# Performance work log

Measured on AMD Instinct MI355X. Metric: run time of the kernel, lower is better.

Reference implementation:

```python
import jax, jax.numpy as jnp
import numpy as np

ZC, ZS = 32, 16
NS = [16384, 4096, 1024, 256, 64]  # mesh node counts per level
K_CH = 6
DEG = 12

def _key(i):
    return jax.random.fold_in(jax.random.key(0), i)

def setup_inputs():
    d = {}
    d["x"] = jax.random.normal(_key(0), (2, 16, NS[0], 3), jnp.float32)
    enc_dims = [(6, 16), (16, 16), (16, 16), (16, 32)]
    dec_dims = [(32, 16), (16, 16), (16, 16), (16, 3)]
    i = 1
    for p, dims in (("enc", enc_dims), ("decc", dec_dims), ("decs", dec_dims)):
        for l, (fi, fo) in enumerate(dims):
            d[p + "_W" + str(l)] = 0.1 * jax.random.normal(_key(i), (K_CH, fi, fo), jnp.float32); i += 1
            if p == "enc" or l < 3:  # last decoder convs have bias=None
                d[p + "_b" + str(l)] = jnp.zeros((fo,), jnp.float32)
    nfz = NS[4] * 32  # _n_features_before_z
    d["mu_W"] = 0.1 * jax.random.normal(_key(i), (ZC + ZS, nfz), jnp.float32); i += 1
    d["mu_b"] = jnp.zeros((ZC + ZS,), jnp.float32)
    d["linc_W"] = 0.1 * jax.random.normal(_key(i), (nfz, ZC), jnp.float32); i += 1
    d["linc_b"] = jnp.zeros((nfz,), jnp.float32)
    d["lins_W"] = 0.1 * jax.random.normal(_key(i), (nfz, ZC + 2 * ZS), jnp.float32); i += 1
    d["lins_b"] = jnp.zeros((nfz,), jnp.float32)
    for l in range(4):
        d["ei" + str(l)] = jax.random.randint(_key(i), (2, DEG * NS[l]), 0, NS[l], jnp.int32); i += 1
    d["ei4"] = jax.random.randint(_key(i), (2, DEG * NS[0]), 0, NS[0], jnp.int32); i += 1
    for l in range(4):
        d["ds_i" + str(l)] = jax.random.randint(_key(i), (NS[l + 1], 3), 0, NS[l], jnp.int32); i += 1
        d["ds_w" + str(l)] = jax.random.uniform(_key(i), (NS[l + 1], 3), jnp.float32); i += 1
        d["us_i" + str(l)] = jax.random.randint(_key(i), (NS[l], 3), 0, NS[l + 1], jnp.int32); i += 1
        d["us_w" + str(l)] = jax.random.uniform(_key(i), (NS[l], 3), jnp.float32); i += 1
    return d

def _norm(ei, n):
    # ChebConv_Coma.norm: D^-1/2 A D^-1/2 edge weights (unit edge weights)
    row, col = ei[0], ei[1]
    deg = jnp.zeros((n,), jnp.float32).at[row].add(1.0)
    dis = jnp.where(deg > 0, 1.0 / jnp.sqrt(jnp.maximum(deg, 1.0)), 0.0)
    return dis[row] * dis[col]

def _prop(x, ei, w, n):
    # sparse matvec: out[:, dst] += w_e * x[:, src]   (x: [B, n, F])
    msg = x[:, ei[0], :] * w[None, :, None]
    return jnp.zeros((x.shape[0], n, x.shape[2]), x.dtype).at[:, ei[1], :].add(msg)

def _cheb(x, ei, w, Wk, b, n):
    # Chebyshev recurrence: T0=x, T1=Lx, Tk=2L T_{k-1} - T_{k-2}
    out = jnp.einsum('bnf,fg->bng', x, Wk[0])
    Tx0 = x
    Tx1 = _prop(x, ei, w, n)
    out = out + jnp.einsum('bnf,fg->bng', Tx1, Wk[1])
    for k in range(2, Wk.shape[0]):
        Tx2 = 2.0 * _prop(Tx1, ei, w, n) - Tx0
        out = out + jnp.einsum('bnf,fg->bng', Tx2, Wk[k])
        Tx0, Tx1 = Tx1, Tx2
    return out if b is None else out + b

def _pool(x, idx, w):
    # sparse pooling matrix, 3 nnz/row: out[:, i] = sum_k w[i,k] * x[:, idx[i,k]]
    return jnp.einsum('bnkf,nk->bnf', x[:, idx, :], w)

def _phase(x):
    # PhaseTensor: doubles last dim with cos/sin phase modulation over time axis 1
    T = x.shape[1]
    th = 2.0 * jnp.pi * jnp.arange(T, dtype=x.dtype) / T
    shp = (1, T) + (1,) * (x.ndim - 2)
    return jnp.concatenate([x * jnp.cos(th).reshape(shp), x * jnp.sin(th).reshape(shp)], axis=-1)

def _model(FL, IL):
    (x, eW0, eb0, eW1, eb1, eW2, eb2, eW3, eb3,
     cW0, cb0, cW1, cb1, cW2, cb2, cW3,
     sW0, sb0, sW1, sb1, sW2, sb2, sW3,
     mu_W, mu_b, linc_W, linc_b, lins_W, lins_b,
     ds_w0, ds_w1, ds_w2, ds_w3, us_w0, us_w1, us_w2, us_w3) = FL
    (ei0, ei1, ei2, ei3, ei4,
     ds_i0, ds_i1, ds_i2, ds_i3, us_i0, us_i1, us_i2, us_i3) = IL
    eis = [ei0, ei1, ei2, ei3, ei4]
    lvl_n = [NS[0], NS[1], NS[2], NS[3], NS[0]]
    nrm = [_norm(eis[l], lvl_n[l]) for l in range(5)]
    B, T, N0, F0 = x.shape
    # phase_input: [B,T,N,3] -> [B,T,N,6]; fold time into batch for the conv stack
    h = _phase(x).reshape(B * T, N0, 2 * F0)
    encW = [(eW0, eb0), (eW1, eb1), (eW2, eb2), (eW3, eb3)]
    dsl = [(ds_i0, ds_w0), (ds_i1, ds_w1), (ds_i2, ds_w2), (ds_i3, ds_w3)]
    usl = [(us_i0, us_w0), (us_i1, us_w1), (us_i2, us_w2), (us_i3, us_w3)]
    for l in range(4):
        h = jax.nn.relu(_cheb(h, eis[l], nrm[l], encW[l][0], encW[l][1], NS[l]))
        h = _pool(h, dsl[l][0], dsl[l][1])
    h = h.reshape(B, T, -1)  # [B, T, N4*32]
    mu = jnp.einsum('btf,zf->btz', h, mu_W) + mu_b
    # faithful to torch code: per-t cat along dim 0 (time-major) then reshape(-1, T, z)
    mu_c = jnp.mean(jnp.swapaxes(mu[..., :ZC], 0, 1).reshape(B, T, ZC), axis=1)
    mu_s = jnp.mean(jnp.swapaxes(mu[..., ZC:], 0, 1).reshape(B, T, ZS), axis=1)

    def dec(z, Ws, bs, lW, lb, relu_first):
        y = z @ lW.T + lb
        if relu_first:
            y = jax.nn.relu(y)
        y = y.reshape(y.shape[0], NS[4], Ws[0].shape[1])  # [*, N4, 32]
        for i in range(3):  # n_layers - 1 upsample+conv+relu
            lvl = 3 - i
            y = _pool(y, usl[lvl][0], usl[lvl][1])
            y = jax.nn.relu(_cheb(y, eis[lvl], nrm[lvl], Ws[i], bs[i], NS[lvl]))
        y = _pool(y, usl[0][0], usl[0][1])
        return _cheb(y, eis[4], nrm[4], Ws[3], None, NS[0])  # final conv, no bias/relu

    s_avg = dec(mu_c, [cW0, cW1, cW2, cW3], [cb0, cb1, cb2], linc_W, linc_b, False)
    # decoder_s, vectorized over timeframes by folding T into batch
    zs_ph = _phase(jnp.broadcast_to(mu_s[:, None, :], (B, T, ZS)))  # [B,T,2*ZS]
    zc_rep = jnp.broadcast_to(mu_c[:, None, :], (B, T, ZC))
    zin = jnp.concatenate([zc_rep, zs_ph], axis=-1).reshape(B * T, ZC + 2 * ZS)
    ds_t = dec(zin, [sW0, sW1, sW2, sW3], [sb0, sb1, sb2], lins_W, lins_b, True).reshape(B, T, N0, 3)
    s_t = s_avg[:, None] + ds_t
    return mu_c, mu_s, s_avg, s_t

def reference(x, enc_W0, enc_b0, enc_W1, enc_b1, enc_W2, enc_b2, enc_W3, enc_b3, decc_W0, decc_b0, decc_W1, decc_b1, decc_W2, decc_b2, decc_W3, decs_W0, decs_b0, decs_W1, decs_b1, decs_W2, decs_b2, decs_W3, mu_W, mu_b, linc_W, linc_b, lins_W, lins_b, ds_w0, ds_w1, ds_w2, ds_w3, us_w0, us_w1, us_w2, us_w3, ei0, ei1, ei2, ei3, ei4, ds_i0, ds_i1, ds_i2, ds_i3, us_i0, us_i1, us_i2, us_i3):
    FL = (x, enc_W0, enc_b0, enc_W1, enc_b1, enc_W2, enc_b2, enc_W3, enc_b3,
          decc_W0, decc_b0, decc_W1, decc_b1, decc_W2, decc_b2, decc_W3,
          decs_W0, decs_b0, decs_W1, decs_b1, decs_W2, decs_b2, decs_W3,
          mu_W, mu_b, linc_W, linc_b, lins_W, lins_b,
          ds_w0, ds_w1, ds_w2, ds_w3, us_w0, us_w1, us_w2, us_w3)
    IL = (ei0, ei1, ei2, ei3, ei4, ds_i0, ds_i1, ds_i2, ds_i3, us_i0, us_i1, us_i2, us_i3)
    return _model(FL, IL)
```

## Files before the change

kernel.cpp:

```cpp
#include <hip/hip_runtime.h>
#include <cstdint>
#include <cstddef>

#define TPB 256

typedef float f32x4 __attribute__((ext_vector_type(4)));
typedef float f32x2 __attribute__((ext_vector_type(2)));
typedef int   i32x4 __attribute__((ext_vector_type(4)));

static inline int cdiv(long long a, int b){ return (int)((a + (long long)b - 1) / b); }

#define NTOT 38144
#define ETOT 457728
#define CTOT 762880
#define RPTOT 38149

static hipStream_t g_s2 = nullptr;
static hipEvent_t g_evF1 = nullptr, g_evPre = nullptr, g_evF2 = nullptr, g_evDecc = nullptr;
__attribute__((constructor)) static void init_side_stream(){
  if (hipStreamCreateWithFlags(&g_s2, hipStreamNonBlocking) != hipSuccess){ g_s2 = nullptr; return; }
  if (hipEventCreateWithFlags(&g_evF1, hipEventDisableTiming) != hipSuccess ||
      hipEventCreateWithFlags(&g_evPre, hipEventDisableTiming) != hipSuccess ||
      hipEventCreateWithFlags(&g_evF2, hipEventDisableTiming) != hipSuccess ||
      hipEventCreateWithFlags(&g_evDecc, hipEventDisableTiming) != hipSuccess){
    g_s2 = nullptr;
  }
}


template<int W>
__device__ __forceinline__ void vload(const float* __restrict__ p, float* r){
  if constexpr (W == 8){ vload<4>(p, r); vload<4>(p+4, r+4); }
  else if constexpr (W == 4){ f32x4 v = *reinterpret_cast<const f32x4*>(p); r[0]=v.x;r[1]=v.y;r[2]=v.z;r[3]=v.w; }
  else { f32x2 v = *reinterpret_cast<const f32x2*>(p); r[0]=v.x;r[1]=v.y; }
}
template<int W>
__device__ __forceinline__ void vstore(float* __restrict__ p, const float* r){
  if constexpr (W == 8){ vstore<4>(p, r); vstore<4>(p+4, r+4); }
  else if constexpr (W == 4){ f32x4 v; v.x=r[0];v.y=r[1];v.z=r[2];v.w=r[3]; *reinterpret_cast<f32x4*>(p) = v; }
  else { f32x2 v; v.x=r[0];v.y=r[1]; *reinterpret_cast<f32x2*>(p) = v; }
}

template<int F>
__device__ __forceinline__ void loadrow(const float* __restrict__ p, float* r){
  #pragma unroll
  for (int q = 0; q < F/4; ++q) vload<4>(p + 4*q, r + 4*q);
}
template<int F>
__device__ __forceinline__ void storerow(float* __restrict__ p, const float* r){
  #pragma unroll
  for (int q = 0; q < F/4; ++q) vstore<4>(p + 4*q, r + 4*q);
}


__device__ __forceinline__ bool lvl_edge(int t, const int* e0,const int* e1,const int* e2,const int* e3,const int* e4,
                                         const int*& ei, int& E, int& noff, int& rpoff, int& rel){
  if (t < 196608){ ei=e0; E=196608; noff=0;     rpoff=0;     rel=t;        return true; }
  if (t < 245760){ ei=e1; E=49152;  noff=16384; rpoff=16385; rel=t-196608; return true; }
  if (t < 258048){ ei=e2; E=12288;  noff=20480; rpoff=20482; rel=t-245760; return true; }
  if (t < 261120){ ei=e3; E=3072;   noff=21504; rpoff=21507; rel=t-258048; return true; }
  if (t < 457728){ ei=e4; E=196608; noff=21760; rpoff=21764; rel=t-261120; return true; }
  return false;
}

__global__ void k_degs_all(const int* e0,const int* e1,const int* e2,const int* e3,const int* e4,
                           int* __restrict__ rowdeg, int* __restrict__ dstdeg){
  int t = blockIdx.x*blockDim.x + threadIdx.x;
  const int* ei; int E, noff, rpoff, rel;
  if (!lvl_edge(t, e0,e1,e2,e3,e4, ei,E,noff,rpoff,rel)) return;
  atomicAdd(&rowdeg[noff + ei[rel]], 1);
  atomicAdd(&dstdeg[noff + ei[E + rel]], 1);
}

__global__ void k_dis_all(const int* __restrict__ rowdeg, float* __restrict__ dis){
  int t = blockIdx.x*blockDim.x + threadIdx.x;
  if (t >= NTOT) return;
  int d = rowdeg[t];
  dis[t] = d > 0 ? rsqrtf((float)d) : 0.f;
}

__global__ void k_scan5(const int* __restrict__ dstdeg, int* __restrict__ rp, int* __restrict__ cursor){
  const int NnA[5]  = {16384,4096,1024,256,16384};
  const int NOFF[5] = {0,16384,20480,21504,21760};
  const int COFF[5] = {0,327680,409600,430080,435200};
  __shared__ int part[257];
  int l = blockIdx.x;
  int N = NnA[l];
  const int* cnt = dstdeg + NOFF[l];
  int* rpl = rp + NOFF[l] + l;
  int* cul = cursor + NOFF[l] + l;
  int tid = threadIdx.x;
  int chunk = (N + 255) / 256;
  int lo = tid*chunk; if (lo > N) lo = N;
  int hi = lo + chunk; if (hi > N) hi = N;
  int s = 0;
  for (int i = lo; i < hi; ++i) s += (cnt[i] + 7) & ~7;
  part[tid+1] = s;
  if (tid == 0) part[0] = COFF[l];
  __syncthreads();
  if (tid == 0){ for (int i = 1; i <= 256; ++i) part[i] += part[i-1]; }
  __syncthreads();
  int run = part[tid];
  for (int i = lo; i < hi; ++i){ rpl[i] = run; cul[i] = run; run += (cnt[i] + 7) & ~7; }
  if (tid == 0) rpl[N] = part[256];
}

__global__ void k_fill_all(const int* e0,const int* e1,const int* e2,const int* e3,const int* e4,
                           const float* __restrict__ dis, int* __restrict__ cursor,
                           int* __restrict__ srcs, float* __restrict__ w){
  int t = blockIdx.x*blockDim.x + threadIdx.x;
  const int* ei; int E, noff, rpoff, rel;
  if (!lvl_edge(t, e0,e1,e2,e3,e4, ei,E,noff,rpoff,rel)) return;
  int src = ei[rel], dst = ei[E + rel];
  int pos = atomicAdd(&cursor[rpoff + dst], 1);
  srcs[pos] = src;
  w[pos] = dis[noff + src] * dis[noff + dst];
}

__global__ void k_pad_all(const int* __restrict__ dstdeg, const int* __restrict__ rp,
                          int* __restrict__ srcs, float* __restrict__ w){
  int t = blockIdx.x*blockDim.x + threadIdx.x;
  if (t >= NTOT) return;
  int rpoff, n;
  if      (t < 16384){ rpoff = 0;     n = t; }
  else if (t < 20480){ rpoff = 16385; n = t - 16384; }
  else if (t < 21504){ rpoff = 20482; n = t - 20480; }
  else if (t < 21760){ rpoff = 21507; n = t - 21504; }
  else               { rpoff = 21764; n = t - 21760; }
  int j0 = rp[rpoff + n];
  int j1 = rp[rpoff + n + 1];
  int cnt = dstdeg[t];
  int sfill = cnt > 0 ? srcs[j0] : 0;
  for (int j = j0 + cnt; j < j1; ++j){ srcs[j] = sfill; w[j] = 0.f; }
}


template<int FinPad>
__device__ __forceinline__ void tmap(int N, int& gb, int& n, int& gs, int& sub, int& laneoff){
  constexpr int LPR = FinPad/4;
  gb = blockIdx.x & 7;
  int I = (blockIdx.x >> 3)*256 + threadIdx.x;
  n = I / FinPad;
  int u = I - n*FinPad;
  gs = u / LPR;
  sub = u - gs*LPR;
  laneoff = gs*FinPad + sub*4;
}

template<int FinPad>
__device__ __forceinline__ void gather8_t(const float* __restrict__ base,
                                          const int* __restrict__ srcs, const float* __restrict__ w,
                                          int j0, int j1, int laneoff, float* acc){
  constexpr int RS = 4*FinPad;
  #pragma unroll
  for (int q = 0; q < 4; ++q) acc[q] = 0.f;
  for (int j = j0; j < j1; j += 8){
    i32x4 sa = *reinterpret_cast<const i32x4*>(srcs + j);
    i32x4 sb = *reinterpret_cast<const i32x4*>(srcs + j + 4);
    f32x4 wa = *reinterpret_cast<const f32x4*>(w + j);
    f32x4 wb = *reinterpret_cast<const f32x4*>(w + j + 4);
    float v0[4], v1[4], v2[4], v3[4], v4[4], v5[4], v6[4], v7[4];
    vload<4>(base + (size_t)sa.x*RS + laneoff, v0);
    vload<4>(base + (size_t)sa.y*RS + laneoff, v1);
    vload<4>(base + (size_t)sa.z*RS + laneoff, v2);
    vload<4>(base + (size_t)sa.w*RS + laneoff, v3);
    vload<4>(base + (size_t)sb.x*RS + laneoff, v4);
    vload<4>(base + (size_t)sb.y*RS + laneoff, v5);
    vload<4>(base + (size_t)sb.z*RS + laneoff, v6);
    vload<4>(base + (size_t)sb.w*RS + laneoff, v7);
    #pragma unroll
    for (int q = 0; q < 4; ++q){
      acc[q] = fmaf(wa.x, v0[q], acc[q]);
      acc[q] = fmaf(wa.y, v1[q], acc[q]);
      acc[q] = fmaf(wa.z, v2[q], acc[q]);
      acc[q] = fmaf(wa.w, v3[q], acc[q]);
      acc[q] = fmaf(wb.x, v4[q], acc[q]);
      acc[q] = fmaf(wb.y, v5[q], acc[q]);
      acc[q] = fmaf(wb.z, v6[q], acc[q]);
      acc[q] = fmaf(wb.w, v7[q], acc[q]);
    }
  }
}

template<int FinPad, int FinReal, int Fout>
__device__ __forceinline__ void gemm_t(const float* ts, const float* __restrict__ Wk,
                                       int sub, float* o){
  constexpr int LPR = FinPad/4;
  int lane = (int)threadIdx.x & 63;
  int lanebase = lane & ~(LPR-1);
  float tv[FinPad];
  #pragma unroll
  for (int s = 0; s < LPR; ++s)
    #pragma unroll
    for (int q = 0; q < 4; ++q)
      tv[s*4+q] = __shfl(ts[q], lanebase + s, 64);
  if constexpr (Fout % 4 == 0){
    constexpr int OPL = Fout/LPR;
    #pragma unroll
    for (int fi = 0; fi < FinReal; ++fi)
      #pragma unroll
      for (int q = 0; q < OPL; ++q)
        o[q] = fmaf(tv[fi], Wk[fi*Fout + sub*OPL + q], o[q]);
  } else {
    if (sub < Fout){
      #pragma unroll
      for (int fi = 0; fi < FinReal; ++fi)
        o[0] = fmaf(tv[fi], Wk[fi*Fout + sub], o[0]);
    }
  }
}

template<int FinPad, int PRE>
__global__ void k_pre_t(const float* __restrict__ psrc, const int* __restrict__ pidx,
                        const float* __restrict__ pw, float* __restrict__ bufX,
                        int N, int Nin){
  int gb, n, gs, sub, laneoff;
  tmap<FinPad>(N, gb, n, gs, sub, laneoff);
  constexpr int RS = 4*FinPad;
  float r[4];
  if constexpr (PRE == 1){
    int g = (gb<<2) | gs;
    int t = g & 15;
    float th = 6.283185307179586f * (float)t / 16.0f;
    float sn, cs; sincosf(th, &sn, &cs);
    const float* xr = psrc + ((size_t)g*16384 + n)*3;
    #pragma unroll
    for (int q = 0; q < 4; ++q){
      int f = sub*4 + q;
      float v = 0.f;
      if (f < 6) v = xr[f % 3] * (f < 3 ? cs : sn);
      r[q] = v;
    }
  } else {
    int i0 = pidx[n*3+0], i1 = pidx[n*3+1], i2 = pidx[n*3+2];
    float w0 = pw[n*3+0], w1 = pw[n*3+1], w2 = pw[n*3+2];
    const float* pb = psrc + (size_t)gb*Nin*RS + laneoff;
    float a[4], b[4], c[4];
    vload<4>(pb + (size_t)i0*RS, a);
    vload<4>(pb + (size_t)i1*RS, b);
    vload<4>(pb + (size_t)i2*RS, c);
    #pragma unroll
    for (int q = 0; q < 4; ++q) r[q] = fmaf(w0, a[q], fmaf(w1, b[q], w2*c[q]));
  }
  vstore<4>(bufX + (size_t)gb*N*RS + (size_t)n*RS + laneoff, r);
}

template<int FinPad, int FinReal, int Fout>
__global__ void k_first_t(const int* __restrict__ rp, const int* __restrict__ srcs, const float* __restrict__ w,
                          const float* __restrict__ bufX, float* __restrict__ bufT1, float* __restrict__ out,
                          const float* __restrict__ W6, const float* __restrict__ bias, int N){
  constexpr int LPR = FinPad/4;
  constexpr int OPL = (Fout % 4 == 0) ? Fout/LPR : 1;
  constexpr int RS = 4*FinPad;
  int gb, n, gs, sub, laneoff;
  tmap<FinPad>(N, gb, n, gs, sub, laneoff);
  const float* gbase = bufX + (size_t)gb*N*RS;
  float t0[4]; vload<4>(gbase + (size_t)n*RS + laneoff, t0);
  float t1[4];
  gather8_t<FinPad>(gbase, srcs, w, rp[n], rp[n+1], laneoff, t1);
  vstore<4>(bufT1 + (size_t)gb*N*RS + (size_t)n*RS + laneoff, t1);
  float o[OPL];
  if constexpr (Fout % 4 == 0){
    #pragma unroll
    for (int q = 0; q < OPL; ++q) o[q] = bias ? bias[sub*OPL + q] : 0.f;
  } else {
    o[0] = (bias && sub < Fout) ? bias[sub] : 0.f;
  }
  gemm_t<FinPad,FinReal,Fout>(t0, W6, sub, o);
  gemm_t<FinPad,FinReal,Fout>(t1, W6 + (size_t)FinReal*Fout, sub, o);
  if constexpr (Fout % 4 == 0){
    vstore<OPL>(out + ((size_t)(gb*N + n)*4 + gs)*Fout + sub*OPL, o);
  } else {
    if (sub < Fout){
      int g = (gb<<2)|gs;
      out[((size_t)g*N + n)*3 + sub] = o[0];
    }
  }
}

template<int FinPad, int FinReal, int Fout>
__global__ void k_step_t(const int* __restrict__ rp, const int* __restrict__ srcs, const float* __restrict__ w,
                         const float* __restrict__ Tm1, float* __restrict__ P, float* __restrict__ out,
                         const float* __restrict__ Wk, const float* __restrict__ savg,
                         int N, int relu, int last){
  constexpr int LPR = FinPad/4;
  constexpr int OPL = (Fout % 4 == 0) ? Fout/LPR : 1;
  constexpr int RS = 4*FinPad;
  int gb, n, gs, sub, laneoff;
  tmap<FinPad>(N, gb, n, gs, sub, laneoff);
  const float* gbase = Tm1 + (size_t)gb*N*RS;
  float tk[4];
  gather8_t<FinPad>(gbase, srcs, w, rp[n], rp[n+1], laneoff, tk);
  float tm2[4]; vload<4>(P + (size_t)gb*N*RS + (size_t)n*RS + laneoff, tm2);
  #pragma unroll
  for (int q = 0; q < 4; ++q) tk[q] = 2.f*tk[q] - tm2[q];
  if (!last) vstore<4>(P + (size_t)gb*N*RS + (size_t)n*RS + laneoff, tk);
  float o[OPL];
  if constexpr (Fout % 4 == 0){
    vload<OPL>(out + ((size_t)(gb*N + n)*4 + gs)*Fout + sub*OPL, o);
  } else {
    o[0] = 0.f;
    if (sub < Fout) o[0] = out[((size_t)((gb<<2)|gs)*N + n)*3 + sub];
  }
  gemm_t<FinPad,FinReal,Fout>(tk, Wk, sub, o);
  if constexpr (Fout % 4 == 0){
    if (last && relu){
      #pragma unroll
      for (int q = 0; q < OPL; ++q) o[q] = fmaxf(o[q], 0.f);
    }
    vstore<OPL>(out + ((size_t)(gb*N + n)*4 + gs)*Fout + sub*OPL, o);
  } else {
    if (sub < Fout){
      float v = o[0];
      if (last && relu) v = fmaxf(v, 0.f);
      int g = (gb<<2)|gs;
      if (last && savg) v += savg[((size_t)(g>>4)*N + n)*3 + sub];
      out[((size_t)g*N + n)*3 + sub] = v;
    }
  }
}


template<int FPL, int FinPad>
__device__ __forceinline__ void gather8(const float* __restrict__ gb,
                                        const int* __restrict__ srcs, const float* __restrict__ w,
                                        int j0, int j1, int sub, float* acc){
  #pragma unroll
  for (int q = 0; q < FPL; ++q) acc[q] = 0.f;
  for (int j = j0; j < j1; j += 8){
    i32x4 sa = *reinterpret_cast<const i32x4*>(srcs + j);
    i32x4 sb = *reinterpret_cast<const i32x4*>(srcs + j + 4);
    f32x4 wa = *reinterpret_cast<const f32x4*>(w + j);
    f32x4 wb = *reinterpret_cast<const f32x4*>(w + j + 4);
    float v0[FPL], v1[FPL], v2[FPL], v3[FPL], v4[FPL], v5[FPL], v6[FPL], v7[FPL];
    vload<FPL>(gb + (size_t)sa.x*FinPad + sub*FPL, v0);
    vload<FPL>(gb + (size_t)sa.y*FinPad + sub*FPL, v1);
    vload<FPL>(gb + (size_t)sa.z*FinPad + sub*FPL, v2);
    vload<FPL>(gb + (size_t)sa.w*FinPad + sub*FPL, v3);
    vload<FPL>(gb + (size_t)sb.x*FinPad + sub*FPL, v4);
    vload<FPL>(gb + (size_t)sb.y*FinPad + sub*FPL, v5);
    vload<FPL>(gb + (size_t)sb.z*FinPad + sub*FPL, v6);
    vload<FPL>(gb + (size_t)sb.w*FinPad + sub*FPL, v7);
    #pragma unroll
    for (int q = 0; q < FPL; ++q){
      acc[q] = fmaf(wa.x, v0[q], acc[q]);
      acc[q] = fmaf(wa.y, v1[q], acc[q]);
      acc[q] = fmaf(wa.z, v2[q], acc[q]);
      acc[q] = fmaf(wa.w, v3[q], acc[q]);
      acc[q] = fmaf(wb.x, v4[q], acc[q]);
      acc[q] = fmaf(wb.y, v5[q], acc[q]);
      acc[q] = fmaf(wb.z, v6[q], acc[q]);
      acc[q] = fmaf(wb.w, v7[q], acc[q]);
    }
  }
}

template<int FinPad, int FinReal, int Fout>
__device__ __forceinline__ void gemm_acc(const float* ts, const float* __restrict__ Wk,
                                         int sub, int lanebase, float* o){
  constexpr int FPL = FinPad/4;
  float tv[FinPad];
  #pragma unroll
  for (int s = 0; s < 4; ++s)
    #pragma unroll
    for (int q = 0; q < FPL; ++q)
      tv[s*FPL+q] = __shfl(ts[q], lanebase + s, 64);
  if constexpr (Fout % 4 == 0){
    constexpr int OPL = Fout/4;
    #pragma unroll
    for (int fi = 0; fi < FinReal; ++fi)
      #pragma unroll
      for (int q = 0; q < OPL; ++q)
        o[q] = fmaf(tv[fi], Wk[fi*Fout + sub*OPL + q], o[q]);
  } else {
    if (sub < Fout){
      #pragma unroll
      for (int fi = 0; fi < FinReal; ++fi)
        o[0] = fmaf(tv[fi], Wk[fi*Fout + sub], o[0]);
    }
  }
}

template<int FinPad>
__global__ void k_pre_f(const float* __restrict__ psrc, const int* __restrict__ pidx,
                        const float* __restrict__ pw, float* __restrict__ bufX,
                        int G, int logN, int Nin){
  constexpr int FPL = FinPad/4;
  long long i4 = (long long)blockIdx.x*blockDim.x + threadIdx.x;
  if (i4 >= ((long long)G << logN)*4) return;
  int sub = (int)(i4 & 3);
  long long i = i4 >> 2;
  int N = 1 << logN;
  int n = (int)(i & (N-1));
  int g = (int)(i >> logN);
  int i0 = pidx[n*3+0], i1 = pidx[n*3+1], i2 = pidx[n*3+2];
  float w0 = pw[n*3+0], w1 = pw[n*3+1], w2 = pw[n*3+2];
  const float* bsrc = psrc + (size_t)g*Nin*FinPad + sub*FPL;
  float a[FPL], b[FPL], c[FPL], r[FPL];
  vload<FPL>(bsrc + (size_t)i0*FinPad, a);
  vload<FPL>(bsrc + (size_t)i1*FinPad, b);
  vload<FPL>(bsrc + (size_t)i2*FinPad, c);
  #pragma unroll
  for (int q = 0; q < FPL; ++q) r[q] = fmaf(w0, a[q], fmaf(w1, b[q], w2*c[q]));
  vstore<FPL>(bufX + (size_t)i*FinPad + sub*FPL, r);
}

template<int FinPad, int FinReal, int Fout>
__global__ void k_first_f(const int* __restrict__ rp, const int* __restrict__ srcs, const float* __restrict__ w,
                          const float* __restrict__ bufX, float* __restrict__ bufT1, float* __restrict__ out,
                          const float* __restrict__ W6, const float* __restrict__ bias,
                          int G, int logN){
  constexpr int FPL = FinPad/4;
  constexpr int OPL = (Fout % 4 == 0) ? Fout/4 : 1;
  long long i4 = (long long)blockIdx.x*blockDim.x + threadIdx.x;
  if (i4 >= ((long long)G << logN)*4) return;
  int sub = (int)(i4 & 3);
  long long i = i4 >> 2;
  int N = 1 << logN;
  int n = (int)(i & (N-1));
  int lanebase = ((int)threadIdx.x & 63) & ~3;
  const float* gb = bufX + (size_t)(i - n)*FinPad;
  float t0[FPL]; vload<FPL>(bufX + (size_t)i*FinPad + sub*FPL, t0);
  float t1[FPL];
  gather8<FPL,FinPad>(gb, srcs, w, rp[n], rp[n+1], sub, t1);
  vstore<FPL>(bufT1 + (size_t)i*FinPad + sub*FPL, t1);
  float o[OPL];
  if constexpr (Fout % 4 == 0){
    #pragma unroll
    for (int q = 0; q < OPL; ++q) o[q] = bias ? bias[sub*OPL + q] : 0.f;
  } else {
    o[0] = (bias && sub < Fout) ? bias[sub] : 0.f;
  }
  gemm_acc<FinPad,FinReal,Fout>(t0, W6, sub, lanebase, o);
  gemm_acc<FinPad,FinReal,Fout>(t1, W6 + (size_t)FinReal*Fout, sub, lanebase, o);
  if constexpr (Fout % 4 == 0) vstore<OPL>(out + (size_t)i*Fout + sub*OPL, o);
  else if (sub < Fout) out[(size_t)i*Fout + sub] = o[0];
}

template<int FinPad, int FinReal, int Fout>
__global__ void k_step_f(const int* __restrict__ rp, const int* __restrict__ srcs, const float* __restrict__ w,
                         const float* __restrict__ Tm1, float* __restrict__ P, float* __restrict__ out,
                         const float* __restrict__ Wk, const float* __restrict__ savg,
                         int G, int logN, int relu, int last){
  constexpr int FPL = FinPad/4;
  constexpr int OPL = (Fout % 4 == 0) ? Fout/4 : 1;
  long long i4 = (long long)blockIdx.x*blockDim.x + threadIdx.x;
  if (i4 >= ((long long)G << logN)*4) return;
  int sub = (int)(i4 & 3);
  long long i = i4 >> 2;
  int N = 1 << logN;
  int n = (int)(i & (N-1));
  int lanebase = ((int)threadIdx.x & 63) & ~3;
  const float* gb = Tm1 + (size_t)(i - n)*FinPad;
  float tk[FPL];
  gather8<FPL,FinPad>(gb, srcs, w, rp[n], rp[n+1], sub, tk);
  float tm2[FPL]; vload<FPL>(P + (size_t)i*FinPad + sub*FPL, tm2);
  #pragma unroll
  for (int q = 0; q < FPL; ++q) tk[q] = 2.f*tk[q] - tm2[q];
  if (!last) vstore<FPL>(P + (size_t)i*FinPad + sub*FPL, tk);
  float o[OPL];
  if constexpr (Fout % 4 == 0) vload<OPL>(out + (size_t)i*Fout + sub*OPL, o);
  else { o[0] = (sub < Fout) ? out[(size_t)i*Fout + sub] : 0.f; }
  gemm_acc<FinPad,FinReal,Fout>(tk, Wk, sub, lanebase, o);
  if constexpr (Fout % 4 == 0){
    if (last && relu){
      #pragma unroll
      for (int q = 0; q < OPL; ++q) o[q] = fmaxf(o[q], 0.f);
    }
    vstore<OPL>(out + (size_t)i*Fout + sub*OPL, o);
  } else {
    if (sub < Fout){
      float v = o[0];
      if (last && relu) v = fmaxf(v, 0.f);
      if (last && savg){
        int g = (int)(i >> logN);
        v += savg[((size_t)(g>>4)*N + n)*3 + sub];
      }
      out[(size_t)i*Fout + sub] = v;
    }
  }
}


__global__ void k_mu_t(const float* __restrict__ h_t, const float* __restrict__ W,
                       const float* __restrict__ b, float* __restrict__ mu){
  int wid = (blockIdx.x*blockDim.x + threadIdx.x) >> 6;
  int lane = threadIdx.x & 63;
  if (wid >= 32*48) return;
  int z = wid % 48, g = wid / 48;
  const float* wr = W + (size_t)z*2048;
  const float* hb = h_t + (size_t)(g>>2)*64*128 + (g&3)*32;
  float acc = 0.f;
  for (int f2 = lane; f2 < 2048; f2 += 64)
    acc = fmaf(hb[(size_t)(f2>>5)*128 + (f2&31)], wr[f2], acc);
  for (int o = 32; o > 0; o >>= 1) acc += __shfl_down(acc, o, 64);
  if (lane == 0) mu[wid] = acc + b[z];
}

__global__ void k_mucs(const float* __restrict__ mu, float* __restrict__ muc,
                       float* __restrict__ mus, float* __restrict__ out){
  int i = blockIdx.x*blockDim.x + threadIdx.x;
  if (i >= 96) return;
  int z = i % 48, bp = i / 48;
  float acc = 0.f;
  for (int b = 0; b < 2; ++b)
    for (int t = 8*bp; t < 8*bp + 8; ++t)
      acc += mu[(b*16 + t)*48 + z];
  acc *= (1.f/16.f);
  if (z < 32){ muc[bp*32 + z] = acc; out[bp*32 + z] = acc; }
  else       { mus[bp*16 + (z-32)] = acc; out[64 + bp*16 + (z-32)] = acc; }
}

__global__ void k_zin(const float* __restrict__ muc, const float* __restrict__ mus,
                      float* __restrict__ zin){
  int i = blockIdx.x*blockDim.x + threadIdx.x;
  if (i >= 32*64) return;
  int c = i % 64, g = i / 64;
  int b = g / 16, t = g % 16;
  float v;
  if (c < 32){
    v = muc[b*32 + c];
  } else {
    float th = 6.283185307179586f * (float)t / 16.0f;
    int k = c - 32;
    int kk = (k < 16) ? k : (k - 16);
    float m = mus[b*16 + kk];
    v = (k < 16) ? m * cosf(th) : m * sinf(th);
  }
  zin[i] = v;
}

__global__ void k_lin(const float* __restrict__ z, const float* __restrict__ W,
                      const float* __restrict__ b, float* __restrict__ y,
                      int G, int Z, int relu){
  int i = blockIdx.x*blockDim.x + threadIdx.x;
  if (i >= G*2048) return;
  int f = i % 2048, g = i / 2048;
  const float* zr = z + (size_t)g*Z;
  const float* wr = W + (size_t)f*Z;
  float acc = b[f];
  for (int k = 0; k < Z; ++k) acc = fmaf(zr[k], wr[k], acc);
  if (relu) acc = fmaxf(acc, 0.f);
  y[i] = acc;
}

__global__ void k_lin_t(const float* __restrict__ z, const float* __restrict__ W,
                        const float* __restrict__ b, float* __restrict__ y_t,
                        int Z, int relu){
  int i = blockIdx.x*blockDim.x + threadIdx.x;
  if (i >= 32*2048) return;
  int f2 = i % 2048, g = i / 2048;
  const float* zr = z + (size_t)g*Z;
  const float* wr = W + (size_t)f2*Z;
  float acc = b[f2];
  for (int k = 0; k < Z; ++k) acc = fmaf(zr[k], wr[k], acc);
  if (relu) acc = fmaxf(acc, 0.f);
  y_t[(size_t)(g>>2)*64*128 + (size_t)(f2>>5)*128 + (g&3)*32 + (f2&31)] = acc;
}


struct LvlArgs {
  const int* rp; const int* srcs; const float* w;
  const float* psrc; const int* pidx; const float* pw;
  float* bufX; float* bufT1; float* out;
  const float* W6; const float* bias; const float* savg;
  int G; int logN; int Nin; int relu;
};

template<int FinPad, int FinReal, int Fout, int PRE>
static void run_level_t(hipStream_t s, const LvlArgs& a, bool do_pre = true){
  int N = 1 << a.logN;
  int grid = 8 * (N*FinPad/256);
  if (do_pre)
    k_pre_t<FinPad,PRE><<<grid,256,0,s>>>(a.psrc, a.pidx, a.pw, a.bufX, N, a.Nin);
  k_first_t<FinPad,FinReal,Fout><<<grid,256,0,s>>>(a.rp, a.srcs, a.w, a.bufX, a.bufT1, a.out,
                                                   a.W6, a.bias, N);
  float* Ab = a.bufT1; float* Bb = a.bufX;
  for (int k = 2; k <= 5; ++k){
    int last = (k == 5) ? 1 : 0;
    k_step_t<FinPad,FinReal,Fout><<<grid,256,0,s>>>(a.rp, a.srcs, a.w, Ab, Bb, a.out,
                                                    a.W6 + (size_t)k*FinReal*Fout,
                                                    last ? a.savg : nullptr,
                                                    N, a.relu, last);
    float* t = Ab; Ab = Bb; Bb = t;
  }
}

template<int FinPad, int FinReal, int Fout>
static void run_level_f(hipStream_t s, const LvlArgs& a){
  long long GN4 = ((long long)a.G << a.logN) * 4;
  int grid = cdiv(GN4, 256);
  k_pre_f<FinPad><<<grid,256,0,s>>>(a.psrc, a.pidx, a.pw, a.bufX, a.G, a.logN, a.Nin);
  k_first_f<FinPad,FinReal,Fout><<<grid,256,0,s>>>(a.rp, a.srcs, a.w, a.bufX, a.bufT1, a.out,
                                                   a.W6, a.bias, a.G, a.logN);
  float* Ab = a.bufT1; float* Bb = a.bufX;
  for (int k = 2; k <= 5; ++k){
    int last = (k == 5) ? 1 : 0;
    k_step_f<FinPad,FinReal,Fout><<<grid,256,0,s>>>(a.rp, a.srcs, a.w, Ab, Bb, a.out,
                                                    a.W6 + (size_t)k*FinReal*Fout,
                                                    last ? a.savg : nullptr,
                                                    a.G, a.logN, a.relu, last);
    float* t = Ab; Ab = Bb; Bb = t;
  }
}

extern "C" void kernel_launch(void* const* d_in, const int* in_sizes, int n_in,
                              void* d_out, int out_size, void* d_ws, size_t ws_size,
                              hipStream_t stream){
  const float* x = (const float*)d_in[0];
  const float* encW[4] = {(const float*)d_in[1],(const float*)d_in[3],(const float*)d_in[5],(const float*)d_in[7]};
  const float* encB[4] = {(const float*)d_in[2],(const float*)d_in[4],(const float*)d_in[6],(const float*)d_in[8]};
  const float* ccW[4]  = {(const float*)d_in[9],(const float*)d_in[11],(const float*)d_in[13],(const float*)d_in[15]};
  const float* ccB[3]  = {(const float*)d_in[10],(const float*)d_in[12],(const float*)d_in[14]};
  const float* csW[4]  = {(const float*)d_in[16],(const float*)d_in[18],(const float*)d_in[20],(const float*)d_in[22]};
  const float* csB[3]  = {(const float*)d_in[17],(const float*)d_in[19],(const float*)d_in[21]};
  const float* muW  = (const float*)d_in[23]; const float* muB  = (const float*)d_in[24];
  const float* lincW = (const float*)d_in[25]; const float* lincB = (const float*)d_in[26];
  const float* linsW = (const float*)d_in[27]; const float* linsB = (const float*)d_in[28];
  const int* ei[5] = {(const int*)d_in[29],(const int*)d_in[30],(const int*)d_in[31],
                      (const int*)d_in[32],(const int*)d_in[33]};
  const int* ds_i[4]; const float* ds_w[4]; const int* us_i[4]; const float* us_w[4];
  for (int l = 0; l < 4; ++l){
    ds_i[l] = (const int*)d_in[34 + 4*l]; ds_w[l] = (const float*)d_in[35 + 4*l];
    us_i[l] = (const int*)d_in[36 + 4*l]; us_w[l] = (const float*)d_in[37 + 4*l];
  }

  float* ws = (float*)d_ws;
  const size_t BIG = 8388608;
  float* B0 = ws + 0*BIG;
  float* B1 = ws + 1*BIG;
  float* B2 = ws + 2*BIG;
  float* B3 = ws + 3*BIG;
  size_t off = 4*BIG;

  int*   rp_all     = (int*)(ws + off); off += RPTOT;
  int*   cursor_all = (int*)(ws + off); off += RPTOT;
  off = (off + 3) & ~(size_t)3;
  int*   srcs_all   = (int*)(ws + off); off += CTOT;
  float* w_all      =        ws + off;  off += CTOT;
  int*   rowdeg     = (int*)(ws + off); off += NTOT;
  int*   dstdeg     = (int*)(ws + off); off += NTOT;
  float* dis        =        ws + off;  off += NTOT;
  float* hmu        =        ws + off;  off += (size_t)32*2048;
  float* mu         =        ws + off;  off += (size_t)32*48;
  float* muc        =        ws + off;  off += 64;
  float* mus        =        ws + off;  off += 32;
  float* zin        =        ws + off;  off += (size_t)32*64;
  const size_t DSM = (size_t)2*16384*16;
  float* D0 = ws + off; off += DSM;
  float* D1 = ws + off; off += DSM;
  float* D2 = ws + off; off += DSM;
  float* D3 = ws + off; off += DSM;

  float* outp = (float*)d_out;
  float* out_savg = outp + 96;
  float* out_st   = outp + 96 + 98304;

  const bool use2 = (g_s2 != nullptr);
  hipStream_t sC = use2 ? g_s2 : stream;

  if (use2){
    hipEventRecord(g_evF1, stream);
    hipStreamWaitEvent(g_s2, g_evF1, 0);
  }
  {
    int N = 16384;
    int grid = 8 * (N*8/256);
    k_pre_t<8,1><<<grid,256,0,sC>>>(x, nullptr, nullptr, B0, N, 0);
    if (use2) hipEventRecord(g_evPre, g_s2);
  }

  hipMemsetAsync(rowdeg, 0, 2*(size_t)NTOT*sizeof(int), stream);
  k_degs_all<<<cdiv(ETOT,TPB),TPB,0,stream>>>(ei[0],ei[1],ei[2],ei[3],ei[4], rowdeg, dstdeg);
  k_dis_all<<<cdiv(NTOT,TPB),TPB,0,stream>>>(rowdeg, dis);
  k_scan5<<<5,256,0,stream>>>(dstdeg, rp_all, cursor_all);
  k_fill_all<<<cdiv(ETOT,TPB),TPB,0,stream>>>(ei[0],ei[1],ei[2],ei[3],ei[4], dis, cursor_all, srcs_all, w_all);
  k_pad_all<<<cdiv(NTOT,TPB),TPB,0,stream>>>(dstdeg, rp_all, srcs_all, w_all);
  if (use2) hipStreamWaitEvent(stream, g_evPre, 0);

  const int RPOFF[5] = {0,16385,20482,21507,21764};
  const int* RP[5];
  for (int l = 0; l < 5; ++l) RP[l] = rp_all + RPOFF[l];

  run_level_t<8,6,16,1>(stream, {RP[0],srcs_all,w_all, x,nullptr,nullptr,
                                 B0,B1,B2, encW[0],encB[0],nullptr, 32,14,0,1}, false);
  run_level_t<16,16,16,0>(stream, {RP[1],srcs_all,w_all, B2,ds_i[0],ds_w[0],
                                   B0,B1,B3, encW[1],encB[1],nullptr, 32,12,16384,1});
  run_level_t<16,16,16,0>(stream, {RP[2],srcs_all,w_all, B3,ds_i[1],ds_w[1],
                                   B0,B1,B2, encW[2],encB[2],nullptr, 32,10,4096,1});
  run_level_t<16,16,32,0>(stream, {RP[3],srcs_all,w_all, B2,ds_i[2],ds_w[2],
                                   B0,B1,B3, encW[3],encB[3],nullptr, 32,8,1024,1});
  {
    int grid = 8 * (64*32/256);
    k_pre_t<32,0><<<grid,256,0,stream>>>(B3, ds_i[3], ds_w[3], hmu, 64, 256);
  }

  k_mu_t<<<cdiv((long long)32*48*64,TPB),TPB,0,stream>>>(hmu, muW, muB, mu);
  k_mucs<<<1,128,0,stream>>>(mu, muc, mus, outp);

  if (use2){
    hipEventRecord(g_evF2, stream);
    hipStreamWaitEvent(g_s2, g_evF2, 0);
  }
  k_lin<<<cdiv((long long)2*2048,TPB),TPB,0,sC>>>(muc, lincW, lincB, D2, 2, 32, 0);
  run_level_f<32,32,16>(sC, {RP[3],srcs_all,w_all, D2,us_i[3],us_w[3],
                             D0,D1,D3, ccW[0],ccB[0],nullptr, 2,8,64,1});
  run_level_f<16,16,16>(sC, {RP[2],srcs_all,w_all, D3,us_i[2],us_w[2],
                             D0,D1,D2, ccW[1],ccB[1],nullptr, 2,10,256,1});
  run_level_f<16,16,16>(sC, {RP[1],srcs_all,w_all, D2,us_i[1],us_w[1],
                             D0,D1,D3, ccW[2],ccB[2],nullptr, 2,12,1024,1});
  run_level_f<16,16,3>(sC, {RP[4],srcs_all,w_all, D3,us_i[0],us_w[0],
                            D0,D1,out_savg, ccW[3],nullptr,nullptr, 2,14,4096,0});
  if (use2) hipEventRecord(g_evDecc, g_s2);

  k_zin<<<cdiv(32*64,TPB),TPB,0,stream>>>(muc, mus, zin);
  k_lin_t<<<cdiv((long long)32*2048,TPB),TPB,0,stream>>>(zin, linsW, linsB, B2, 64, 1);
  run_level_t<32,32,16,0>(stream, {RP[3],srcs_all,w_all, B2,us_i[3],us_w[3],
                                   B0,B1,B3, csW[0],csB[0],nullptr, 32,8,64,1});
  run_level_t<16,16,16,0>(stream, {RP[2],srcs_all,w_all, B3,us_i[2],us_w[2],
                                   B0,B1,B2, csW[1],csB[1],nullptr, 32,10,256,1});
  run_level_t<16,16,16,0>(stream, {RP[1],srcs_all,w_all, B2,us_i[1],us_w[1],
                                   B0,B1,B3, csW[2],csB[2],nullptr, 32,12,1024,1});
  if (use2) hipStreamWaitEvent(stream, g_evDecc, 0);
  run_level_t<16,16,3,0>(stream, {RP[4],srcs_all,w_all, B3,us_i[0],us_w[0],
                                  B0,B1,out_st, csW[3],nullptr,out_savg, 32,14,4096,0});

  (void)in_sizes; (void)n_in; (void)out_size; (void)ws_size;
}
```

Before: 1.125 ms.

## Fuse small-level Chebyshev convolutions into single-block LDS-resident kernels

Adds a per-graph kernel that holds a whole small mesh level (256 or 1024 nodes) in shared memory and runs the pooling gather, all six Chebyshev recurrence steps and the weight GEMM in one launch, using __syncthreads between steps instead of separate kernel launches and global round-trips. The encoder's last pooling and the content decoder's linear layer plus its first two levels are fused into the same style of kernel. This is meant to remove launch overhead and global-memory traffic on the tiny levels. In exchange each kernel runs only 32 (or 2) blocks with large LDS use, so parallelism is low and everything depends on one CU per graph.

```diff
diff --git a/kernel.cpp b/kernel.cpp
--- a/kernel.cpp
+++ b/kernel.cpp
@@ -321,6 +321,192 @@
 }
 
 
+template<int Fin, int SP>
+__device__ __forceinline__ void gth_sh(const float* __restrict__ T,
+                                       const int* __restrict__ srcs, const float* __restrict__ w,
+                                       int j0, int j1, float* acc){
+  #pragma unroll
+  for (int f = 0; f < Fin; ++f) acc[f] = 0.f;
+  for (int j = j0; j < j1; ++j){
+    float ww = w[j];
+    const float* r = T + srcs[j]*SP;
+    #pragma unroll
+    for (int q = 0; q < Fin/2; ++q){
+      f32x2 v = *reinterpret_cast<const f32x2*>(r + 2*q);
+      acc[2*q]   = fmaf(ww, v.x, acc[2*q]);
+      acc[2*q+1] = fmaf(ww, v.y, acc[2*q+1]);
+    }
+  }
+}
+
+template<int Fin, int Fout>
+__device__ __forceinline__ void gemm_full(const float* t, const float* __restrict__ Wk, float* o){
+  #pragma unroll
+  for (int fi = 0; fi < Fin; ++fi){
+    float tv = t[fi];
+    #pragma unroll
+    for (int fo = 0; fo < Fout; ++fo)
+      o[fo] = fmaf(tv, Wk[fi*Fout + fo], o[fo]);
+  }
+}
+
+template<int N, int Fin, int Fout, bool RELU>
+__device__ __forceinline__ void cheb_core_sh(float* A, float* B,
+                                             const int* __restrict__ rp,
+                                             const int* __restrict__ srcs, const float* __restrict__ w,
+                                             const float* __restrict__ W6, const float* __restrict__ bias,
+                                             int tid, float* o){
+  constexpr int SP = Fin + 2;
+  int j0 = 0, j1 = 0;
+  if (tid < N){ j0 = rp[tid]; j1 = rp[tid+1]; }
+  if (tid < N){
+    float t0[Fin], t1[Fin];
+    #pragma unroll
+    for (int f = 0; f < Fin; ++f) t0[f] = A[tid*SP + f];
+    gth_sh<Fin,SP>(A, srcs, w, j0, j1, t1);
+    #pragma unroll
+    for (int f = 0; f < Fin; ++f) B[tid*SP + f] = t1[f];
+    #pragma unroll
+    for (int fo = 0; fo < Fout; ++fo) o[fo] = bias ? bias[fo] : 0.f;
+    gemm_full<Fin,Fout>(t0, W6, o);
+    gemm_full<Fin,Fout>(t1, W6 + Fin*Fout, o);
+  }
+  __syncthreads();
+  float* X = B; float* Y = A;
+  for (int kk = 2; kk <= 5; ++kk){
+    const float* Wk = W6 + kk*Fin*Fout;
+    if (tid < N){
+      float tk[Fin];
+      gth_sh<Fin,SP>(X, srcs, w, j0, j1, tk);
+      #pragma unroll
+      for (int f = 0; f < Fin; ++f) tk[f] = 2.f*tk[f] - Y[tid*SP + f];
+      if (kk < 5){
+        #pragma unroll
+        for (int f = 0; f < Fin; ++f) Y[tid*SP + f] = tk[f];
+      }
+      gemm_full<Fin,Fout>(tk, Wk, o);
+    }
+    __syncthreads();
+    float* t = X; X = Y; Y = t;
+  }
+  if (RELU && tid < N){
+    #pragma unroll
+    for (int fo = 0; fo < Fout; ++fo) o[fo] = fmaxf(o[fo], 0.f);
+  }
+}
+
+template<int N, int Fin, int Fout, int EPI>
+__global__ void __launch_bounds__(N, 1)
+k_cheb_lds(const int* __restrict__ rp, const int* __restrict__ srcs, const float* __restrict__ w,
+           const float* __restrict__ psrc, const int* __restrict__ pidx, const float* __restrict__ pw,
+           int Nin,
+           float* __restrict__ out_t, const float* __restrict__ W6, const float* __restrict__ bias,
+           const int* __restrict__ eidx, const float* __restrict__ ew, float* __restrict__ eout){
+  constexpr int SP = Fin + 2;
+  extern __shared__ float smem[];
+  float* A = smem;
+  float* B = smem + N*SP;
+  float* O = smem + 2*N*SP;
+  int gb = blockIdx.x & 7, gs = blockIdx.x >> 3;
+  int tid = threadIdx.x;
+  {
+    int n = tid;
+    int i0 = pidx[n*3+0], i1 = pidx[n*3+1], i2 = pidx[n*3+2];
+    float w0 = pw[n*3+0], w1 = pw[n*3+1], w2 = pw[n*3+2];
+    const float* pb = psrc + (size_t)gb*Nin*4*Fin + (size_t)gs*Fin;
+    #pragma unroll
+    for (int q = 0; q < Fin/4; ++q){
+      float a[4], b[4], c[4];
+      vload<4>(pb + (size_t)i0*4*Fin + 4*q, a);
+      vload<4>(pb + (size_t)i1*4*Fin + 4*q, b);
+      vload<4>(pb + (size_t)i2*4*Fin + 4*q, c);
+      #pragma unroll
+      for (int e = 0; e < 4; ++e)
+        A[n*SP + 4*q + e] = fmaf(w0, a[e], fmaf(w1, b[e], w2*c[e]));
+    }
+  }
+  __syncthreads();
+  float o[Fout];
+  cheb_core_sh<N,Fin,Fout,true>(A, B, rp, srcs, w, W6, bias, tid, o);
+  if constexpr (EPI == 0){
+    float* op = out_t + ((size_t)(gb*N + tid)*4 + gs)*Fout;
+    #pragma unroll
+    for (int q = 0; q < Fout/4; ++q) vstore<4>(op + 4*q, o + 4*q);
+  } else {
+    constexpr int SO = Fout + 2;
+    #pragma unroll
+    for (int f = 0; f < Fout; ++f) O[tid*SO + f] = o[f];
+    __syncthreads();
+    if (tid < 64){
+      int i0 = eidx[tid*3+0], i1 = eidx[tid*3+1], i2 = eidx[tid*3+2];
+      float w0 = ew[tid*3+0], w1 = ew[tid*3+1], w2 = ew[tid*3+2];
+      float r[32];
+      #pragma unroll
+      for (int f = 0; f < 32; ++f)
+        r[f] = fmaf(w0, O[i0*SO+f], fmaf(w1, O[i1*SO+f], w2*O[i2*SO+f]));
+      float* hp = eout + (size_t)gb*8192 + (size_t)tid*128 + gs*32;
+      #pragma unroll
+      for (int q = 0; q < 8; ++q) vstore<4>(hp + 4*q, r + 4*q);
+    }
+  }
+}
+
+__global__ void __launch_bounds__(1024, 1)
+k_decc_head(const float* __restrict__ muc,
+            const float* __restrict__ lW, const float* __restrict__ lb,
+            const int* __restrict__ rp3, const int* __restrict__ rp2,
+            const int* __restrict__ srcs, const float* __restrict__ w,
+            const int* __restrict__ ui3, const float* __restrict__ uw3,
+            const int* __restrict__ ui2, const float* __restrict__ uw2,
+            const float* __restrict__ Wa, const float* __restrict__ ba,
+            const float* __restrict__ Wb, const float* __restrict__ bb,
+            float* __restrict__ outD){
+  extern __shared__ float smem[];
+  float* Y = smem;
+  float* A = smem + 2048;
+  float* B = A + 1024*18;
+  int g = blockIdx.x, tid = threadIdx.x;
+  const float* z = muc + g*32;
+  for (int f = tid; f < 2048; f += 1024){
+    float acc = lb[f];
+    const float* wr = lW + (size_t)f*32;
+    #pragma unroll
+    for (int k = 0; k < 32; ++k) acc = fmaf(z[k], wr[k], acc);
+    Y[f] = acc;
+  }
+  __syncthreads();
+  if (tid < 256){
+    int i0 = ui3[tid*3+0], i1 = ui3[tid*3+1], i2 = ui3[tid*3+2];
+    float w0 = uw3[tid*3+0], w1 = uw3[tid*3+1], w2 = uw3[tid*3+2];
+    #pragma unroll
+    for (int f = 0; f < 32; ++f)
+      A[tid*34 + f] = fmaf(w0, Y[i0*32+f], fmaf(w1, Y[i1*32+f], w2*Y[i2*32+f]));
+  }
+  __syncthreads();
+  float oa[16];
+  cheb_core_sh<256,32,16,true>(A, B, rp3, srcs, w, Wa, ba, tid, oa);
+  float* O = B + 256*34;
+  if (tid < 256){
+    #pragma unroll
+    for (int f = 0; f < 16; ++f) O[tid*18 + f] = oa[f];
+  }
+  __syncthreads();
+  {
+    int i0 = ui2[tid*3+0], i1 = ui2[tid*3+1], i2 = ui2[tid*3+2];
+    float w0 = uw2[tid*3+0], w1 = uw2[tid*3+1], w2 = uw2[tid*3+2];
+    #pragma unroll
+    for (int f = 0; f < 16; ++f)
+      A[tid*18 + f] = fmaf(w0, O[i0*18+f], fmaf(w1, O[i1*18+f], w2*O[i2*18+f]));
+  }
+  __syncthreads();
+  float ob[16];
+  cheb_core_sh<1024,16,16,true>(A, B, rp2, srcs, w, Wb, bb, tid, ob);
+  float* op = outD + ((size_t)g*1024 + tid)*16;
+  #pragma unroll
+  for (int q = 0; q < 4; ++q) vstore<4>(op + 4*q, ob + 4*q);
+}
+
+
 template<int FPL, int FinPad>
 __device__ __forceinline__ void gather8(const float* __restrict__ gb,
                                         const int* __restrict__ srcs, const float* __restrict__ w,
@@ -530,20 +716,6 @@
   zin[i] = v;
 }
 
-__global__ void k_lin(const float* __restrict__ z, const float* __restrict__ W,
-                      const float* __restrict__ b, float* __restrict__ y,
-                      int G, int Z, int relu){
-  int i = blockIdx.x*blockDim.x + threadIdx.x;
-  if (i >= G*2048) return;
-  int f = i % 2048, g = i / 2048;
-  const float* zr = z + (size_t)g*Z;
-  const float* wr = W + (size_t)f*Z;
-  float acc = b[f];
-  for (int k = 0; k < Z; ++k) acc = fmaf(zr[k], wr[k], acc);
-  if (relu) acc = fmaxf(acc, 0.f);
-  y[i] = acc;
-}
-
 __global__ void k_lin_t(const float* __restrict__ z, const float* __restrict__ W,
                         const float* __restrict__ b, float* __restrict__ y_t,
                         int Z, int relu){
@@ -682,18 +854,19 @@
   const int* RP[5];
   for (int l = 0; l < 5; ++l) RP[l] = rp_all + RPOFF[l];
 
+  const int SM_L2 = 2*1024*18*4;
+  const int SM_L3E = (2*256*18 + 256*34)*4;
+  const int SM_L3S = 2*256*34*4;
+  const int SM_HEAD = (2048 + 2*1024*18)*4;
+
   run_level_t<8,6,16,1>(stream, {RP[0],srcs_all,w_all, x,nullptr,nullptr,
                                  B0,B1,B2, encW[0],encB[0],nullptr, 32,14,0,1}, false);
   run_level_t<16,16,16,0>(stream, {RP[1],srcs_all,w_all, B2,ds_i[0],ds_w[0],
                                    B0,B1,B3, encW[1],encB[1],nullptr, 32,12,16384,1});
-  run_level_t<16,16,16,0>(stream, {RP[2],srcs_all,w_all, B3,ds_i[1],ds_w[1],
-                                   B0,B1,B2, encW[2],encB[2],nullptr, 32,10,4096,1});
-  run_level_t<16,16,32,0>(stream, {RP[3],srcs_all,w_all, B2,ds_i[2],ds_w[2],
-                                   B0,B1,B3, encW[3],encB[3],nullptr, 32,8,1024,1});
-  {
-    int grid = 8 * (64*32/256);
-    k_pre_t<32,0><<<grid,256,0,stream>>>(B3, ds_i[3], ds_w[3], hmu, 64, 256);
-  }
+  k_cheb_lds<1024,16,16,0><<<32,1024,SM_L2,stream>>>(RP[2], srcs_all, w_all,
+      B3, ds_i[1], ds_w[1], 4096, B2, encW[2], encB[2], nullptr, nullptr, nullptr);
+  k_cheb_lds<256,16,32,1><<<32,256,SM_L3E,stream>>>(RP[3], srcs_all, w_all,
+      B2, ds_i[2], ds_w[2], 1024, nullptr, encW[3], encB[3], ds_i[3], ds_w[3], hmu);
 
   k_mu_t<<<cdiv((long long)32*48*64,TPB),TPB,0,stream>>>(hmu, muW, muB, mu);
   k_mucs<<<1,128,0,stream>>>(mu, muc, mus, outp);
@@ -702,11 +875,9 @@
     hipEventRecord(g_evF2, stream);
     hipStreamWaitEvent(g_s2, g_evF2, 0);
   }
-  k_lin<<<cdiv((long long)2*2048,TPB),TPB,0,sC>>>(muc, lincW, lincB, D2, 2, 32, 0);
-  run_level_f<32,32,16>(sC, {RP[3],srcs_all,w_all, D2,us_i[3],us_w[3],
-                             D0,D1,D3, ccW[0],ccB[0],nullptr, 2,8,64,1});
-  run_level_f<16,16,16>(sC, {RP[2],srcs_all,w_all, D3,us_i[2],us_w[2],
-                             D0,D1,D2, ccW[1],ccB[1],nullptr, 2,10,256,1});
+  k_decc_head<<<2,1024,SM_HEAD,sC>>>(muc, lincW, lincB, RP[3], RP[2], srcs_all, w_all,
+                                     us_i[3], us_w[3], us_i[2], us_w[2],
+                                     ccW[0], ccB[0], ccW[1], ccB[1], D2);
   run_level_f<16,16,16>(sC, {RP[1],srcs_all,w_all, D2,us_i[1],us_w[1],
                              D0,D1,D3, ccW[2],ccB[2],nullptr, 2,12,1024,1});
   run_level_f<16,16,3>(sC, {RP[4],srcs_all,w_all, D3,us_i[0],us_w[0],
@@ -715,10 +886,10 @@
 
   k_zin<<<cdiv(32*64,TPB),TPB,0,stream>>>(muc, mus, zin);
   k_lin_t<<<cdiv((long long)32*2048,TPB),TPB,0,stream>>>(zin, linsW, linsB, B2, 64, 1);
-  run_level_t<32,32,16,0>(stream, {RP[3],srcs_all,w_all, B2,us_i[3],us_w[3],
-                                   B0,B1,B3, csW[0],csB[0],nullptr, 32,8,64,1});
-  run_level_t<16,16,16,0>(stream, {RP[2],srcs_all,w_all, B3,us_i[2],us_w[2],
-                                   B0,B1,B2, csW[1],csB[1],nullptr, 32,10,256,1});
+  k_cheb_lds<256,32,16,0><<<32,256,SM_L3S,stream>>>(RP[3], srcs_all, w_all,
+      B2, us_i[3], us_w[3], 64, B3, csW[0], csB[0], nullptr, nullptr, nullptr);
+  k_cheb_lds<1024,16,16,0><<<32,1024,SM_L2,stream>>>(RP[2], srcs_all, w_all,
+      B3, us_i[2], us_w[2], 256, B2, csW[1], csB[1], nullptr, nullptr, nullptr);
   run_level_t<16,16,16,0>(stream, {RP[1],srcs_all,w_all, B2,us_i[1],us_w[1],
                                    B0,B1,B3, csW[2],csB[2],nullptr, 32,12,1024,1});
   if (use2) hipStreamWaitEvent(stream, g_evDecc, 0);
```

Measured after the change: 1.220 ms. +8.5%, slower.
